# Performance work log

Hardware: AMD Instinct MI355X
Metric: run time of the kernel (lower is better)

## Reference

```python
import jax, jax.numpy as jnp
import numpy as np

N, NFEAT, NHID, NCLASS, H1 = 4096, 512, 64, 16, 8
GAIN = 1.414  # xavier gain used by the torch module
NEG_SLOPE = 0.2
MASK_VAL = -1e10


def _xavier(k, shape):
    fan_in, fan_out = shape[-2], shape[-1]
    lim = GAIN * (6.0 / (fan_in + fan_out)) ** 0.5
    return jax.random.uniform(k, shape, jnp.float32, -lim, lim)


def setup_inputs() -> dict:
    key = jax.random.key(0)
    ks = jax.random.split(key, 10)
    return {
        "x": jax.random.normal(ks[0], (N, NFEAT), jnp.float32),
        "adj": jax.random.randint(ks[1], (N, N), 0, 2, jnp.int32),
        # layer-1 parameters, stacked over H1 heads
        "W1": _xavier(ks[2], (H1, NFEAT, NHID)),
        "b1": jnp.zeros((H1, NHID), jnp.float32),
        "as1": _xavier(ks[3], (H1, NHID, 1))[..., 0],
        "an1": _xavier(ks[4], (H1, NHID, 1))[..., 0],
        # layer-2 parameters (single head, input = H1*NHID due to concat)
        "W2": _xavier(ks[5], (H1 * NHID, NCLASS)),
        "b2": jnp.zeros((NCLASS,), jnp.float32),
        "as2": _xavier(ks[6], (NCLASS, 1))[:, 0],
        "an2": _xavier(ks[7], (NCLASS, 1))[:, 0],
    }


def gat_layer(X, adj_pos, W, b, a_s, a_n):
    # X: [N, Fin], W: [Fin, Fout], a_s/a_n: [Fout], adj_pos: [N, N] bool
    feats = X @ W                                        # [N, Fout]
    s = feats @ a_s                                      # [N]
    nb = feats @ a_n                                     # [N]
    attn = jax.nn.leaky_relu(s[:, None] + nb[None, :], NEG_SLOPE)  # [N, N]
    attn = jnp.where(adj_pos, attn, MASK_VAL)
    attn = jax.nn.softmax(attn, axis=-1)
    # dropout on attn/feats is a no-op in eval mode
    return attn @ feats + b                              # [N, Fout]


def reference(x, adj, W1, b1, as1, an1, W2, b2, as2, an2):
    adj_pos = adj > 0
    # x dropout is a no-op in eval mode
    layer1 = jax.vmap(gat_layer, in_axes=(None, None, 0, 0, 0, 0))
    h = jax.nn.relu(layer1(x, adj_pos, W1, b1, as1, an1))    # [H1, N, NHID]
    h = jnp.transpose(h, (1, 0, 2)).reshape(N, H1 * NHID)    # concat heads on dim 1
    h = jax.nn.elu(h)
    out = jax.nn.relu(gat_layer(h, adj_pos, W2, b2, as2, an2))  # [N, NCLASS]
    return jax.nn.log_softmax(out, axis=1)
```

## Files before the change

### kernel.cpp

```cpp
#include <hip/hip_runtime.h>

#define NN 4096
#define NFEAT 512
#define NHID 64
#define H1 8
#define NCLS 16
#define BND 40.0f
#define VSTR 72

typedef short bf16x8 __attribute__((ext_vector_type(8)));
typedef float f32x4 __attribute__((ext_vector_type(4)));

__device__ __forceinline__ unsigned short f2bf(float f) {
    unsigned u = __float_as_uint(f);
    u += 0x7fffu + ((u >> 16) & 1u);
    return (unsigned short)(u >> 16);
}
__device__ __forceinline__ float leaky(float v) { return fmaxf(v, 0.2f * v); }
__device__ __forceinline__ unsigned pkbf(float lo, float hi) {
    return __builtin_amdgcn_perm(__float_as_uint(hi) + 0x8000u,
                                 __float_as_uint(lo) + 0x8000u, 0x07060302u);
}
__device__ __forceinline__ bf16x8 mk8(unsigned a, unsigned b, unsigned c, unsigned d) {
    union { unsigned u[4]; bf16x8 v; } cv;
    cv.u[0] = a; cv.u[1] = b; cv.u[2] = c; cv.u[3] = d; return cv.v;
}

__global__ __launch_bounds__(256)
void k_prep(const int* __restrict__ adj, unsigned long long* __restrict__ bits,
            const float* __restrict__ W1, unsigned short* __restrict__ w1f)
{
    __shared__ float wt[64][65];
    const int t = threadIdx.x, bx = blockIdx.x;
    if (bx < NN) {
        const int wv = t >> 6, lane = t & 63;
        const int* ap = adj + (size_t)bx * NN;
        for (int w = wv; w < 64; w += 4) {
            unsigned long long m = __ballot(ap[w * 64 + lane] > 0);
            if (lane == 0) bits[(size_t)bx * 64 + w] = m;
        }
        return;
    }
    const int kt = (bx - NN) & 7, h = (bx - NN) >> 3;
    #pragma unroll
    for (int i = 0; i < 4; ++i) {
        const int f = t + 256 * i;
        const int r = f >> 4, c4 = f & 15;
        const float4 v = *(const float4*)(W1 + ((size_t)(h * NFEAT) + kt * 64 + r) * NHID + c4 * 4);
        wt[r][c4 * 4 + 0] = v.x; wt[r][c4 * 4 + 1] = v.y;
        wt[r][c4 * 4 + 2] = v.z; wt[r][c4 * 4 + 3] = v.w;
    }
    __syncthreads();
    #pragma unroll
    for (int s = 0; s < 2; ++s) {
        const int o = t + s * 256;
        const int kg2 = o >> 8, rem = o & 255;
        const int nt = rem >> 6, lane2 = rem & 63;
        const int qq = lane2 >> 4, nn = lane2 & 15;
        const int kl = kg2 * 32 + qq * 8;
        const int c = nt * 16 + nn;
        uint4 w;
        w.x = pkbf(wt[kl + 0][c], wt[kl + 1][c]);
        w.y = pkbf(wt[kl + 2][c], wt[kl + 3][c]);
        w.z = pkbf(wt[kl + 4][c], wt[kl + 5][c]);
        w.w = pkbf(wt[kl + 6][c], wt[kl + 7][c]);
        *(uint4*)(w1f + (((size_t)h * 16 + kt * 2 + kg2) * 4 + nt) * 512 + lane2 * 8) = w;
    }
}

__global__ __launch_bounds__(256)
void k_feats1(const float* __restrict__ x, const unsigned short* __restrict__ w1f,
              const float* __restrict__ as1, const float* __restrict__ an1,
              unsigned short* __restrict__ f1bT, float* __restrict__ s1,
              float* __restrict__ F1a, float* __restrict__ F2a)
{
    const int t = threadIdx.x, wv = t >> 6, lane = t & 63;
    const int q = lane >> 4, n = lane & 15;
    const int h = blockIdx.y, R0 = blockIdx.x * 64;
    const int row = R0 + wv * 16 + n;
    const float* ap = x + (size_t)row * NFEAT;
    const unsigned short* wp = w1f + (size_t)h * 16 * 4 * 512 + lane * 8;
    f32x4 acc[4] = {{0.f,0.f,0.f,0.f},{0.f,0.f,0.f,0.f},{0.f,0.f,0.f,0.f},{0.f,0.f,0.f,0.f}};
    #pragma unroll 4
    for (int kg = 0; kg < 16; ++kg) {
        const float4 xa = *(const float4*)(ap + kg * 32 + q * 8);
        const float4 xb = *(const float4*)(ap + kg * 32 + q * 8 + 4);
        const bf16x8 af = mk8(pkbf(xa.x, xa.y), pkbf(xa.z, xa.w),
                              pkbf(xb.x, xb.y), pkbf(xb.z, xb.w));
        #pragma unroll
        for (int nt = 0; nt < 4; ++nt) {
            const bf16x8 bf = *(const bf16x8*)(wp + (size_t)(kg * 4 + nt) * 512);
            acc[nt] = __builtin_amdgcn_mfma_f32_16x16x32_bf16(af, bf, acc[nt], 0, 0, 0);
        }
    }
    #pragma unroll
    for (int nt = 0; nt < 4; ++nt) {
        uint2 w;
        w.x = pkbf(acc[nt][0], acc[nt][1]);
        w.y = pkbf(acc[nt][2], acc[nt][3]);
        *(uint2*)(f1bT + ((size_t)h * NHID + nt * 16 + n) * NN + R0 + wv * 16 + q * 4) = w;
    }
    float asv[4], anv[4];
    #pragma unroll
    for (int nt = 0; nt < 4; ++nt) {
        asv[nt] = as1[h * NHID + nt * 16 + n];
        anv[nt] = an1[h * NHID + nt * 16 + n];
    }
    #pragma unroll
    for (int i = 0; i < 4; ++i) {
        float ps = acc[0][i]*asv[0] + acc[1][i]*asv[1] + acc[2][i]*asv[2] + acc[3][i]*asv[3];
        float pn = acc[0][i]*anv[0] + acc[1][i]*anv[1] + acc[2][i]*anv[2] + acc[3][i]*anv[3];
        #pragma unroll
        for (int off = 8; off > 0; off >>= 1) {
            ps += __shfl_xor(ps, off, 64);
            pn += __shfl_xor(pn, off, 64);
        }
        if (n == 0) {
            const int idx = R0 + wv * 16 + q * 4 + i;
            s1[h * NN + idx] = ps;
            F1a[h * NN + idx] = __expf(pn - BND);
            F2a[h * NN + idx] = __expf(0.2f * (pn - BND));
        }
    }
}

__global__ __launch_bounds__(512, 4)
void k_gat1(const unsigned short* __restrict__ f1bT, const float* __restrict__ s1,
            const float* __restrict__ F1, const float* __restrict__ F2,
            const unsigned long long* __restrict__ abits, const float* __restrict__ b1,
            unsigned short* __restrict__ hcatb)
{
    __shared__ __align__(16) char smem[4 * 2 * 64 * VSTR * 2];
    unsigned short* vT = (unsigned short*)smem;

    const int t = threadIdx.x, wv = t >> 6, lane = t & 63;
    const int q = lane >> 4, n = lane & 15;
    const int rg = wv >> 2, jq = wv & 3;
    const int h = blockIdx.y, R0 = blockIdx.x * 64;
    const int rowA = R0 + rg * 32 + n;
    const int rowB = rowA + 16;
    const float vA = s1[h * NN + rowA] + BND, mhA = leaky(vA);
    const float vB = s1[h * NN + rowB] + BND, mhB = leaky(vB);
    const float E1A = __expf(vA - mhA), E2A = __expf(0.2f * vA - mhA);
    const float E1B = __expf(vB - mhB), E2B = __expf(0.2f * vB - mhB);
    const unsigned long long* arowA = abits + (size_t)rowA * 64;
    const unsigned long long* arowB = abits + (size_t)rowB * 64;
    const float* F1p = F1 + (size_t)h * NN;
    const float* F2p = F2 + (size_t)h * NN;

    const int stile = t >> 7;
    const int sc0 = (t & 127) >> 3, sj8 = t & 7;
    const unsigned short* sbase = f1bT + (size_t)h * NHID * NN + (size_t)sc0 * NN + sj8 * 8;
    const int dof = sc0 * VSTR + sj8 * 8;

    f32x4 accA[4] = {{0.f,0.f,0.f,0.f},{0.f,0.f,0.f,0.f},{0.f,0.f,0.f,0.f},{0.f,0.f,0.f,0.f}};
    f32x4 accB[4] = {{0.f,0.f,0.f,0.f},{0.f,0.f,0.f,0.f},{0.f,0.f,0.f,0.f},{0.f,0.f,0.f,0.f}};
    float lsA = 0.f, lsB = 0.f;

    {
        const int js = stile * 1024;
        int4 v0 = *(const int4*)(sbase + js);
        int4 v1 = *(const int4*)(sbase + (size_t)16 * NN + js);
        int4 v2 = *(const int4*)(sbase + (size_t)32 * NN + js);
        int4 v3 = *(const int4*)(sbase + (size_t)48 * NN + js);
        unsigned short* d = vT + (stile * 2 + 0) * (64 * VSTR) + dof;
        *(int4*)(d) = v0;
        *(int4*)(d + 16 * VSTR) = v1;
        *(int4*)(d + 32 * VSTR) = v2;
        *(int4*)(d + 48 * VSTR) = v3;
    }
    __syncthreads();

    for (int it = 0; it < 16; ++it) {
        const int db = it & 1;
        int4 p0, p1, p2, p3;
        if (it < 15) {
            const int js = stile * 1024 + (it + 1) * 64;
            p0 = *(const int4*)(sbase + js);
            p1 = *(const int4*)(sbase + (size_t)16 * NN + js);
            p2 = *(const int4*)(sbase + (size_t)32 * NN + js);
            p3 = *(const int4*)(sbase + (size_t)48 * NN + js);
        }
        const int j0 = jq * 1024 + it * 64;
        const unsigned long long aA = arowA[j0 >> 6];
        const unsigned long long aB = arowB[j0 >> 6];
        const unsigned short* tbase = vT + (jq * 2 + db) * (64 * VSTR);
        #pragma unroll
        for (int ch = 0; ch < 2; ++ch) {
            const int kb = ch * 32 + q * 8;
            const float4 f1a = *(const float4*)(F1p + j0 + kb);
            const float4 f1b = *(const float4*)(F1p + j0 + kb + 4);
            const float4 f2a = *(const float4*)(F2p + j0 + kb);
            const float4 f2b = *(const float4*)(F2p + j0 + kb + 4);
            const float F1v[8] = {f1a.x, f1a.y, f1a.z, f1a.w, f1b.x, f1b.y, f1b.z, f1b.w};
            const float F2v[8] = {f2a.x, f2a.y, f2a.z, f2a.w, f2b.x, f2b.y, f2b.z, f2b.w};
            const unsigned bA = (unsigned)(aA >> kb) & 0xffu;
            const unsigned bB = (unsigned)(aB >> kb) & 0xffu;
            unsigned uA[4], uB[4];
            #pragma unroll
            for (int jp = 0; jp < 4; ++jp) {
                float a0 = fmaxf(E1A * F1v[2*jp],   E2A * F2v[2*jp]);
                float a1 = fmaxf(E1A * F1v[2*jp+1], E2A * F2v[2*jp+1]);
                a0 = ((bA >> (2*jp)) & 1u) ? a0 : 0.f;
                a1 = ((bA >> (2*jp+1)) & 1u) ? a1 : 0.f;
                lsA += a0 + a1;
                uA[jp] = pkbf(a0, a1);
                float b0 = fmaxf(E1B * F1v[2*jp],   E2B * F2v[2*jp]);
                float b1v = fmaxf(E1B * F1v[2*jp+1], E2B * F2v[2*jp+1]);
                b0 = ((bB >> (2*jp)) & 1u) ? b0 : 0.f;
                b1v = ((bB >> (2*jp+1)) & 1u) ? b1v : 0.f;
                lsB += b0 + b1v;
                uB[jp] = pkbf(b0, b1v);
            }
            const bf16x8 afA = mk8(uA[0], uA[1], uA[2], uA[3]);
            const bf16x8 afB = mk8(uB[0], uB[1], uB[2], uB[3]);
            #pragma unroll
            for (int nt = 0; nt < 4; ++nt) {
                const bf16x8 bf = *(const bf16x8*)(tbase + (nt * 16 + n) * VSTR + kb);
                accA[nt] = __builtin_amdgcn_mfma_f32_16x16x32_bf16(afA, bf, accA[nt], 0, 0, 0);
                accB[nt] = __builtin_amdgcn_mfma_f32_16x16x32_bf16(afB, bf, accB[nt], 0, 0, 0);
            }
        }
        if (it < 15) {
            unsigned short* d = vT + (stile * 2 + (db ^ 1)) * (64 * VSTR) + dof;
            *(int4*)(d) = p0;
            *(int4*)(d + 16 * VSTR) = p1;
            *(int4*)(d + 32 * VSTR) = p2;
            *(int4*)(d + 48 * VSTR) = p3;
        }
        __syncthreads();
    }

    lsA += __shfl_xor(lsA, 16, 64); lsA += __shfl_xor(lsA, 32, 64);
    lsB += __shfl_xor(lsB, 16, 64); lsB += __shfl_xor(lsB, 32, 64);

    float* cmbf = (float*)smem;
    float* lwf  = (float*)(smem + 69632);
    #pragma unroll
    for (int nt = 0; nt < 4; ++nt)
        #pragma unroll
        for (int i = 0; i < 4; ++i) {
            cmbf[((size_t)jq * 64 + rg * 32 + q * 4 + i) * 68 + nt * 16 + n] = accA[nt][i];
            cmbf[((size_t)jq * 64 + rg * 32 + 16 + q * 4 + i) * 68 + nt * 16 + n] = accB[nt][i];
        }
    if (q == 0) {
        lwf[jq * 64 + rg * 32 + n] = lsA;
        lwf[jq * 64 + rg * 32 + 16 + n] = lsB;
    }
    __syncthreads();

    const int col = t & 63, r8 = t >> 6;
    const float bv = b1[h * NHID + col];
    #pragma unroll
    for (int rr = 0; rr < 8; ++rr) {
        const int r = r8 * 8 + rr;
        float tot = 0.f, lt = 0.f;
        #pragma unroll
        for (int jj = 0; jj < 4; ++jj) {
            tot += cmbf[((size_t)jj * 64 + r) * 68 + col];
            lt  += lwf[jj * 64 + r];
        }
        hcatb[(size_t)(R0 + r) * (H1 * NHID) + h * NHID + col] =
            f2bf(fmaxf(tot / lt + bv, 0.f));
    }
}

__global__ __launch_bounds__(128)
void k_feats2(const unsigned short* __restrict__ hcatb, const float* __restrict__ W2,
              const float* __restrict__ as2, const float* __restrict__ an2,
              unsigned short* __restrict__ f2bT, float* __restrict__ s2,
              float* __restrict__ F1b, float* __restrict__ F2b)
{
    __shared__ __align__(16) unsigned short w2T[NCLS][520];
    const int t = threadIdx.x, wv = t >> 6, lane = t & 63;
    const int q = lane >> 4, n = lane & 15;
    #pragma unroll
    for (int i = 0; i < 16; ++i) {
        const int f4 = t + 128 * i;
        const float4 v = ((const float4*)W2)[f4];
        const int k = f4 >> 2, c0 = (f4 & 3) * 4;
        w2T[c0 + 0][k] = f2bf(v.x); w2T[c0 + 1][k] = f2bf(v.y);
        w2T[c0 + 2][k] = f2bf(v.z); w2T[c0 + 3][k] = f2bf(v.w);
    }
    __syncthreads();

    const int R0 = blockIdx.x * 32;
    const int row = R0 + wv * 16 + n;
    const unsigned short* ap = hcatb + (size_t)row * NFEAT;
    f32x4 acc = {0.f, 0.f, 0.f, 0.f};
    #pragma unroll 4
    for (int k0 = 0; k0 < NFEAT; k0 += 32) {
        const bf16x8 af = *(const bf16x8*)(ap + k0 + q * 8);
        const bf16x8 bf = *(const bf16x8*)&w2T[n][k0 + q * 8];
        acc = __builtin_amdgcn_mfma_f32_16x16x32_bf16(af, bf, acc, 0, 0, 0);
    }
    uint2 w;
    w.x = pkbf(acc[0], acc[1]);
    w.y = pkbf(acc[2], acc[3]);
    *(uint2*)(f2bT + (size_t)n * NN + R0 + wv * 16 + q * 4) = w;
    const float asv = as2[n], anv = an2[n];
    #pragma unroll
    for (int i = 0; i < 4; ++i) {
        float ps = acc[i] * asv, pn = acc[i] * anv;
        #pragma unroll
        for (int off = 8; off > 0; off >>= 1) {
            ps += __shfl_xor(ps, off, 64);
            pn += __shfl_xor(pn, off, 64);
        }
        if (n == 0) {
            const int idx = R0 + wv * 16 + q * 4 + i;
            s2[idx] = ps;
            F1b[idx] = __expf(pn - BND);
            F2b[idx] = __expf(0.2f * (pn - BND));
        }
    }
}

__global__ __launch_bounds__(1024)
void k_gat2(const unsigned short* __restrict__ f2bT, const float* __restrict__ s2,
            const float* __restrict__ F1, const float* __restrict__ F2,
            const unsigned long long* __restrict__ abits, const float* __restrict__ b2,
            float* __restrict__ out)
{
    __shared__ float cmb[16][16][17];
    __shared__ float lw[16][16];
    const int t = threadIdx.x, wv = t >> 6, lane = t & 63;
    const int q = lane >> 4, n = lane & 15;
    const int R0 = blockIdx.x * 16, row = R0 + n;
    const float v = s2[row] + BND, mhat = leaky(v);
    const float E1 = __expf(v - mhat), E2 = __expf(0.2f * v - mhat);
    const unsigned long long* arow = abits + (size_t)row * 64;

    f32x4 acc = {0.f, 0.f, 0.f, 0.f};
    float lsum = 0.f;
    const int jbeg = wv * 256;
    for (int j0 = jbeg; j0 < jbeg + 256; j0 += 64) {
        const unsigned long long a64 = arow[j0 >> 6];
        #pragma unroll
        for (int ch = 0; ch < 2; ++ch) {
            const int kb = ch * 32 + q * 8;
            const float4 f1a = *(const float4*)(F1 + j0 + kb);
            const float4 f1b = *(const float4*)(F1 + j0 + kb + 4);
            const float4 f2a = *(const float4*)(F2 + j0 + kb);
            const float4 f2b = *(const float4*)(F2 + j0 + kb + 4);
            const float F1v[8] = {f1a.x, f1a.y, f1a.z, f1a.w, f1b.x, f1b.y, f1b.z, f1b.w};
            const float F2v[8] = {f2a.x, f2a.y, f2a.z, f2a.w, f2b.x, f2b.y, f2b.z, f2b.w};
            const unsigned b8 = (unsigned)(a64 >> kb) & 0xffu;
            unsigned au[4];
            #pragma unroll
            for (int jp = 0; jp < 4; ++jp) {
                float p0 = fmaxf(E1 * F1v[2*jp],   E2 * F2v[2*jp]);
                float p1 = fmaxf(E1 * F1v[2*jp+1], E2 * F2v[2*jp+1]);
                p0 = ((b8 >> (2*jp)) & 1u) ? p0 : 0.f;
                p1 = ((b8 >> (2*jp+1)) & 1u) ? p1 : 0.f;
                lsum += p0 + p1;
                au[jp] = pkbf(p0, p1);
            }
            const bf16x8 af = mk8(au[0], au[1], au[2], au[3]);
            const bf16x8 bf = *(const bf16x8*)(f2bT + (size_t)n * NN + j0 + kb);
            acc = __builtin_amdgcn_mfma_f32_16x16x32_bf16(af, bf, acc, 0, 0, 0);
        }
    }
    lsum += __shfl_xor(lsum, 16, 64);
    lsum += __shfl_xor(lsum, 32, 64);
    #pragma unroll
    for (int i = 0; i < 4; ++i) cmb[wv][q * 4 + i][n] = acc[i];
    if (q == 0) lw[wv][n] = lsum;
    __syncthreads();

    if (t < 256) {
        const int r = t >> 4, c = t & 15;
        float tot = 0.f, lt = 0.f;
        #pragma unroll
        for (int w16 = 0; w16 < 16; ++w16) { tot += cmb[w16][r][c]; lt += lw[w16][r]; }
        float val = fmaxf(tot / lt + b2[c], 0.f);
        float mx = val;
        #pragma unroll
        for (int off = 1; off < 16; off <<= 1) mx = fmaxf(mx, __shfl_xor(mx, off, 64));
        const float e = __expf(val - mx);
        float se = e;
        #pragma unroll
        for (int off = 1; off < 16; off <<= 1) se += __shfl_xor(se, off, 64);
        out[(size_t)(R0 + r) * NCLS + c] = val - mx - __logf(se);
    }
}

extern "C" void kernel_launch(void* const* d_in, const int* in_sizes, int n_in,
                              void* d_out, int out_size, void* d_ws, size_t ws_size,
                              hipStream_t stream)
{
    const float* x   = (const float*)d_in[0];
    const int*   adj = (const int*)  d_in[1];
    const float* W1  = (const float*)d_in[2];
    const float* b1  = (const float*)d_in[3];
    const float* as1 = (const float*)d_in[4];
    const float* an1 = (const float*)d_in[5];
    const float* W2  = (const float*)d_in[6];
    const float* b2  = (const float*)d_in[7];
    const float* as2 = (const float*)d_in[8];
    const float* an2 = (const float*)d_in[9];
    float* out = (float*)d_out;

    char* ws = (char*)d_ws;
    unsigned long long* abits = (unsigned long long*)(ws);
    unsigned short* f1bT  = (unsigned short*)(ws + (2u << 20));
    unsigned short* hcatb = (unsigned short*)(ws + (6u << 20));
    unsigned short* w1f   = (unsigned short*)(ws + (10u << 20));
    char* ws2 = ws + (10u << 20) + (512u << 10);
    float* s1   = (float*)(ws2);
    float* F1a  = (float*)(ws2 + (128u << 10));
    float* F2a  = (float*)(ws2 + (256u << 10));
    unsigned short* f2bT = (unsigned short*)(ws2 + (384u << 10));
    float* s2   = (float*)(ws2 + (512u << 10));
    float* F1b  = (float*)(ws2 + (528u << 10));
    float* F2b  = (float*)(ws2 + (544u << 10));

    k_prep  <<<dim3(NN + 64),     256, 0, stream>>>(adj, abits, W1, w1f);
    k_feats1<<<dim3(NN / 64, H1), 256, 0, stream>>>(x, w1f, as1, an1, f1bT, s1, F1a, F2a);
    k_gat1  <<<dim3(NN / 64, H1), 512, 0, stream>>>(f1bT, s1, F1a, F2a, abits, b1, hcatb);
    k_feats2<<<dim3(NN / 32),     128, 0, stream>>>(hcatb, W2, as2, an2, f2bT, s2, F1b, F2b);
    k_gat2  <<<dim3(NN / 16),     1024, 0, stream>>>(f2bT, s2, F1b, F2b, abits, b2, out);
}
```

Before: 209.8 us.

## Switch layer-1 attention to packed fp16 math with per-head max-shifted exponent factors

Layer 1 now uses fp16 instead of bf16 for inputs, weights, features and attention probabilities. It computes attention weights with packed half2 multiply/max and masks them by multiplying with 0/1 constants. x is converted to fp16 once in the prep kernel, and a new per-head kernel rescales the neighbour exponent factors by the per-head max and stores them as fp16 scaled by a constant. The aim is to halve the ALU work and load bandwidth in the inner attention loop and the global loads in the feature GEMM, at the cost of an extra small launch, reduced fp16 range and precision risk, and an 8-block kernel that runs with little parallelism.

```diff
diff --git a/kernel.cpp b/kernel.cpp
--- a/kernel.cpp
+++ b/kernel.cpp
@@ -7,8 +7,12 @@
 #define NCLS 16
 #define BND 40.0f
 #define VSTR 72
+#define FSCL 4096.0f
 
 typedef short bf16x8 __attribute__((ext_vector_type(8)));
+typedef _Float16 f16x8 __attribute__((ext_vector_type(8)));
+typedef _Float16 h2 __attribute__((ext_vector_type(2)));
+typedef __fp16 fp16v2 __attribute__((ext_vector_type(2)));
 typedef float f32x4 __attribute__((ext_vector_type(4)));
 
 __device__ __forceinline__ unsigned short f2bf(float f) {
@@ -21,14 +25,26 @@
     return __builtin_amdgcn_perm(__float_as_uint(hi) + 0x8000u,
                                  __float_as_uint(lo) + 0x8000u, 0x07060302u);
 }
+__device__ __forceinline__ unsigned pkh(float lo, float hi) {
+    union { fp16v2 h; unsigned u; } c;
+    c.h = __builtin_amdgcn_cvt_pkrtz(lo, hi);
+    return c.u;
+}
+__device__ __forceinline__ h2 uash(unsigned u) { union { unsigned u; h2 h; } c; c.u = u; return c.h; }
+__device__ __forceinline__ unsigned hasu(h2 h) { union { unsigned u; h2 h; } c; c.h = h; return c.u; }
 __device__ __forceinline__ bf16x8 mk8(unsigned a, unsigned b, unsigned c, unsigned d) {
     union { unsigned u[4]; bf16x8 v; } cv;
     cv.u[0] = a; cv.u[1] = b; cv.u[2] = c; cv.u[3] = d; return cv.v;
 }
+__device__ __forceinline__ f16x8 mk8h(unsigned a, unsigned b, unsigned c, unsigned d) {
+    union { unsigned u[4]; f16x8 v; } cv;
+    cv.u[0] = a; cv.u[1] = b; cv.u[2] = c; cv.u[3] = d; return cv.v;
+}
 
 __global__ __launch_bounds__(256)
 void k_prep(const int* __restrict__ adj, unsigned long long* __restrict__ bits,
-            const float* __restrict__ W1, unsigned short* __restrict__ w1f)
+            const float* __restrict__ W1, unsigned short* __restrict__ w1f,
+            const float* __restrict__ x, unsigned short* __restrict__ xh)
 {
     __shared__ float wt[64][65];
     const int t = threadIdx.x, bx = blockIdx.x;
@@ -41,6 +57,17 @@
         }
         return;
     }
+    if (bx >= NN + 64) {
+        const int b = bx - NN - 64;
+        #pragma unroll
+        for (int i = 0; i < 4; ++i) {
+            const int f4 = b * 1024 + i * 256 + t;
+            const float4 v = ((const float4*)x)[f4];
+            uint2 w; w.x = pkh(v.x, v.y); w.y = pkh(v.z, v.w);
+            ((uint2*)xh)[f4] = w;
+        }
+        return;
+    }
     const int kt = (bx - NN) & 7, h = (bx - NN) >> 3;
     #pragma unroll
     for (int i = 0; i < 4; ++i) {
@@ -60,44 +87,40 @@
         const int kl = kg2 * 32 + qq * 8;
         const int c = nt * 16 + nn;
         uint4 w;
-        w.x = pkbf(wt[kl + 0][c], wt[kl + 1][c]);
-        w.y = pkbf(wt[kl + 2][c], wt[kl + 3][c]);
-        w.z = pkbf(wt[kl + 4][c], wt[kl + 5][c]);
-        w.w = pkbf(wt[kl + 6][c], wt[kl + 7][c]);
+        w.x = pkh(wt[kl + 0][c], wt[kl + 1][c]);
+        w.y = pkh(wt[kl + 2][c], wt[kl + 3][c]);
+        w.z = pkh(wt[kl + 4][c], wt[kl + 5][c]);
+        w.w = pkh(wt[kl + 6][c], wt[kl + 7][c]);
         *(uint4*)(w1f + (((size_t)h * 16 + kt * 2 + kg2) * 4 + nt) * 512 + lane2 * 8) = w;
     }
 }
 
 __global__ __launch_bounds__(256)
-void k_feats1(const float* __restrict__ x, const unsigned short* __restrict__ w1f,
+void k_feats1(const unsigned short* __restrict__ xh, const unsigned short* __restrict__ w1f,
               const float* __restrict__ as1, const float* __restrict__ an1,
-              unsigned short* __restrict__ f1bT, float* __restrict__ s1,
-              float* __restrict__ F1a, float* __restrict__ F2a)
+              unsigned short* __restrict__ f1bT, float* __restrict__ s1, float* __restrict__ nb1)
 {
     const int t = threadIdx.x, wv = t >> 6, lane = t & 63;
     const int q = lane >> 4, n = lane & 15;
     const int h = blockIdx.y, R0 = blockIdx.x * 64;
     const int row = R0 + wv * 16 + n;
-    const float* ap = x + (size_t)row * NFEAT;
+    const unsigned short* ap = xh + (size_t)row * NFEAT;
     const unsigned short* wp = w1f + (size_t)h * 16 * 4 * 512 + lane * 8;
     f32x4 acc[4] = {{0.f,0.f,0.f,0.f},{0.f,0.f,0.f,0.f},{0.f,0.f,0.f,0.f},{0.f,0.f,0.f,0.f}};
     #pragma unroll 4
     for (int kg = 0; kg < 16; ++kg) {
-        const float4 xa = *(const float4*)(ap + kg * 32 + q * 8);
-        const float4 xb = *(const float4*)(ap + kg * 32 + q * 8 + 4);
-        const bf16x8 af = mk8(pkbf(xa.x, xa.y), pkbf(xa.z, xa.w),
-                              pkbf(xb.x, xb.y), pkbf(xb.z, xb.w));
+        const f16x8 af = *(const f16x8*)(ap + kg * 32 + q * 8);
         #pragma unroll
         for (int nt = 0; nt < 4; ++nt) {
-            const bf16x8 bf = *(const bf16x8*)(wp + (size_t)(kg * 4 + nt) * 512);
-            acc[nt] = __builtin_amdgcn_mfma_f32_16x16x32_bf16(af, bf, acc[nt], 0, 0, 0);
+            const f16x8 bf = *(const f16x8*)(wp + (size_t)(kg * 4 + nt) * 512);
+            acc[nt] = __builtin_amdgcn_mfma_f32_16x16x32_f16(af, bf, acc[nt], 0, 0, 0);
         }
     }
     #pragma unroll
     for (int nt = 0; nt < 4; ++nt) {
         uint2 w;
-        w.x = pkbf(acc[nt][0], acc[nt][1]);
-        w.y = pkbf(acc[nt][2], acc[nt][3]);
+        w.x = pkh(acc[nt][0], acc[nt][1]);
+        w.y = pkh(acc[nt][2], acc[nt][3]);
         *(uint2*)(f1bT + ((size_t)h * NHID + nt * 16 + n) * NN + R0 + wv * 16 + q * 4) = w;
     }
     float asv[4], anv[4];
@@ -118,17 +141,43 @@
         if (n == 0) {
             const int idx = R0 + wv * 16 + q * 4 + i;
             s1[h * NN + idx] = ps;
-            F1a[h * NN + idx] = __expf(pn - BND);
-            F2a[h * NN + idx] = __expf(0.2f * (pn - BND));
-        }
+            nb1[h * NN + idx] = pn;
+        }
+    }
+}
+
+__global__ __launch_bounds__(256)
+void k_fact1(const float* __restrict__ nb1, unsigned short* __restrict__ F1h,
+             unsigned short* __restrict__ F2h, float* __restrict__ nbmax)
+{
+    const int b = blockIdx.x, t = threadIdx.x;
+    const float* p = nb1 + (size_t)b * NN;
+    float m = -INFINITY;
+    for (int i = t; i < NN; i += 256) m = fmaxf(m, p[i]);
+    #pragma unroll
+    for (int off = 32; off > 0; off >>= 1) m = fmaxf(m, __shfl_xor(m, off, 64));
+    __shared__ float sm[4];
+    __shared__ float smx;
+    if ((t & 63) == 0) sm[t >> 6] = m;
+    __syncthreads();
+    if (t == 0) {
+        const float mm = fmaxf(fmaxf(sm[0], sm[1]), fmaxf(sm[2], sm[3]));
+        smx = mm; nbmax[b] = mm;
+    }
+    __syncthreads();
+    const float mx = smx;
+    for (int i = t * 2; i < NN; i += 512) {
+        const float d0 = p[i] - mx, d1 = p[i + 1] - mx;
+        ((unsigned*)F1h)[((size_t)b * NN + i) >> 1] = pkh(FSCL * __expf(d0), FSCL * __expf(d1));
+        ((unsigned*)F2h)[((size_t)b * NN + i) >> 1] = pkh(FSCL * __expf(0.2f * d0), FSCL * __expf(0.2f * d1));
     }
 }
 
 __global__ __launch_bounds__(512, 4)
 void k_gat1(const unsigned short* __restrict__ f1bT, const float* __restrict__ s1,
-            const float* __restrict__ F1, const float* __restrict__ F2,
+            const unsigned short* __restrict__ F1h, const unsigned short* __restrict__ F2h,
             const unsigned long long* __restrict__ abits, const float* __restrict__ b1,
-            unsigned short* __restrict__ hcatb)
+            const float* __restrict__ nbmax1, unsigned short* __restrict__ hcatb)
 {
     __shared__ __align__(16) char smem[4 * 2 * 64 * VSTR * 2];
     unsigned short* vT = (unsigned short*)smem;
@@ -139,14 +188,19 @@
     const int h = blockIdx.y, R0 = blockIdx.x * 64;
     const int rowA = R0 + rg * 32 + n;
     const int rowB = rowA + 16;
-    const float vA = s1[h * NN + rowA] + BND, mhA = leaky(vA);
-    const float vB = s1[h * NN + rowB] + BND, mhB = leaky(vB);
-    const float E1A = __expf(vA - mhA), E2A = __expf(0.2f * vA - mhA);
-    const float E1B = __expf(vB - mhB), E2B = __expf(0.2f * vB - mhB);
+    const float mh = nbmax1[h];
+    const float vA = s1[h * NN + rowA] + mh, mhA = leaky(vA);
+    const float vB = s1[h * NN + rowB] + mh, mhB = leaky(vB);
+    const float E1Af = __expf(vA - mhA), E2Af = __expf(0.2f * vA - mhA);
+    const float E1Bf = __expf(vB - mhB), E2Bf = __expf(0.2f * vB - mhB);
+    const h2 E1A = {(_Float16)E1Af, (_Float16)E1Af};
+    const h2 E2A = {(_Float16)E2Af, (_Float16)E2Af};
+    const h2 E1B = {(_Float16)E1Bf, (_Float16)E1Bf};
+    const h2 E2B = {(_Float16)E2Bf, (_Float16)E2Bf};
     const unsigned long long* arowA = abits + (size_t)rowA * 64;
     const unsigned long long* arowB = abits + (size_t)rowB * 64;
-    const float* F1p = F1 + (size_t)h * NN;
-    const float* F2p = F2 + (size_t)h * NN;
+    const unsigned short* F1p = F1h + (size_t)h * NN;
+    const unsigned short* F2p = F2h + (size_t)h * NN;
 
     const int stile = t >> 7;
     const int sc0 = (t & 127) >> 3, sj8 = t & 7;
@@ -188,37 +242,35 @@
         #pragma unroll
         for (int ch = 0; ch < 2; ++ch) {
             const int kb = ch * 32 + q * 8;
-            const float4 f1a = *(const float4*)(F1p + j0 + kb);
-            const float4 f1b = *(const float4*)(F1p + j0 + kb + 4);
-            const float4 f2a = *(const float4*)(F2p + j0 + kb);
-            const float4 f2b = *(const float4*)(F2p + j0 + kb + 4);
-            const float F1v[8] = {f1a.x, f1a.y, f1a.z, f1a.w, f1b.x, f1b.y, f1b.z, f1b.w};
-            const float F2v[8] = {f2a.x, f2a.y, f2a.z, f2a.w, f2b.x, f2b.y, f2b.z, f2b.w};
+            const uint4 f1w = *(const uint4*)(F1p + j0 + kb);
+            const uint4 f2w = *(const uint4*)(F2p + j0 + kb);
             const unsigned bA = (unsigned)(aA >> kb) & 0xffu;
             const unsigned bB = (unsigned)(aB >> kb) & 0xffu;
             unsigned uA[4], uB[4];
+            h2 sA2 = {(_Float16)0, (_Float16)0};
+            h2 sB2 = {(_Float16)0, (_Float16)0};
             #pragma unroll
             for (int jp = 0; jp < 4; ++jp) {
-                float a0 = fmaxf(E1A * F1v[2*jp],   E2A * F2v[2*jp]);
-                float a1 = fmaxf(E1A * F1v[2*jp+1], E2A * F2v[2*jp+1]);
-                a0 = ((bA >> (2*jp)) & 1u) ? a0 : 0.f;
-                a1 = ((bA >> (2*jp+1)) & 1u) ? a1 : 0.f;
-                lsA += a0 + a1;
-                uA[jp] = pkbf(a0, a1);
-                float b0 = fmaxf(E1B * F1v[2*jp],   E2B * F2v[2*jp]);
-                float b1v = fmaxf(E1B * F1v[2*jp+1], E2B * F2v[2*jp+1]);
-                b0 = ((bB >> (2*jp)) & 1u) ? b0 : 0.f;
-                b1v = ((bB >> (2*jp+1)) & 1u) ? b1v : 0.f;
-                lsB += b0 + b1v;
-                uB[jp] = pkbf(b0, b1v);
+                const h2 f1 = uash(((const unsigned*)&f1w)[jp]);
+                const h2 f2 = uash(((const unsigned*)&f2w)[jp]);
+                const unsigned mA = ((bA >> (2*jp)) & 1u) * 0x3C00u
+                                  + ((bA >> (2*jp+1)) & 1u) * 0x3C000000u;
+                const unsigned mB = ((bB >> (2*jp)) & 1u) * 0x3C00u
+                                  + ((bB >> (2*jp+1)) & 1u) * 0x3C000000u;
+                h2 pA = __builtin_elementwise_max(E1A * f1, E2A * f2) * uash(mA);
+                h2 pB = __builtin_elementwise_max(E1B * f1, E2B * f2) * uash(mB);
+                sA2 += pA; sB2 += pB;
+                uA[jp] = hasu(pA); uB[jp] = hasu(pB);
             }
-            const bf16x8 afA = mk8(uA[0], uA[1], uA[2], uA[3]);
-            const bf16x8 afB = mk8(uB[0], uB[1], uB[2], uB[3]);
+            lsA += (float)sA2[0] + (float)sA2[1];
+            lsB += (float)sB2[0] + (float)sB2[1];
+            const f16x8 afA = mk8h(uA[0], uA[1], uA[2], uA[3]);
+            const f16x8 afB = mk8h(uB[0], uB[1], uB[2], uB[3]);
             #pragma unroll
             for (int nt = 0; nt < 4; ++nt) {
-                const bf16x8 bf = *(const bf16x8*)(tbase + (nt * 16 + n) * VSTR + kb);
-                accA[nt] = __builtin_amdgcn_mfma_f32_16x16x32_bf16(afA, bf, accA[nt], 0, 0, 0);
-                accB[nt] = __builtin_amdgcn_mfma_f32_16x16x32_bf16(afB, bf, accB[nt], 0, 0, 0);
+                const f16x8 bf = *(const f16x8*)(tbase + (nt * 16 + n) * VSTR + kb);
+                accA[nt] = __builtin_amdgcn_mfma_f32_16x16x32_f16(afA, bf, accA[nt], 0, 0, 0);
+                accB[nt] = __builtin_amdgcn_mfma_f32_16x16x32_f16(afB, bf, accB[nt], 0, 0, 0);
             }
         }
         if (it < 15) {
@@ -404,20 +456,24 @@
     char* ws = (char*)d_ws;
     unsigned long long* abits = (unsigned long long*)(ws);
     unsigned short* f1bT  = (unsigned short*)(ws + (2u << 20));
-    unsigned short* hcatb = (unsigned short*)(ws + (6u << 20));
+    unsigned short* xh    = (unsigned short*)(ws + (6u << 20));
+    unsigned short* hcatb = xh;
     unsigned short* w1f   = (unsigned short*)(ws + (10u << 20));
     char* ws2 = ws + (10u << 20) + (512u << 10);
     float* s1   = (float*)(ws2);
-    float* F1a  = (float*)(ws2 + (128u << 10));
-    float* F2a  = (float*)(ws2 + (256u << 10));
+    float* nb1  = (float*)(ws2 + (128u << 10));
+    unsigned short* F1h = (unsigned short*)(ws2 + (256u << 10));
+    unsigned short* F2h = (unsigned short*)(ws2 + (320u << 10));
     unsigned short* f2bT = (unsigned short*)(ws2 + (384u << 10));
     float* s2   = (float*)(ws2 + (512u << 10));
     float* F1b  = (float*)(ws2 + (528u << 10));
     float* F2b  = (float*)(ws2 + (544u << 10));
-
-    k_prep  <<<dim3(NN + 64),     256, 0, stream>>>(adj, abits, W1, w1f);
-    k_feats1<<<dim3(NN / 64, H1), 256, 0, stream>>>(x, w1f, as1, an1, f1bT, s1, F1a, F2a);
-    k_gat1  <<<dim3(NN / 64, H1), 512, 0, stream>>>(f1bT, s1, F1a, F2a, abits, b1, hcatb);
-    k_feats2<<<dim3(NN / 32),     128, 0, stream>>>(hcatb, W2, as2, an2, f2bT, s2, F1b, F2b);
-    k_gat2  <<<dim3(NN / 16),     1024, 0, stream>>>(f2bT, s2, F1b, F2b, abits, b2, out);
-}
+    float* nbmax1 = (float*)(ws2 + (560u << 10));
+
+    k_prep  <<<dim3(NN + 64 + 512), 256, 0, stream>>>(adj, abits, W1, w1f, x, xh);
+    k_feats1<<<dim3(NN / 64, H1),   256, 0, stream>>>(xh, w1f, as1, an1, f1bT, s1, nb1);
+    k_fact1 <<<dim3(H1),            256, 0, stream>>>(nb1, F1h, F2h, nbmax1);
+    k_gat1  <<<dim3(NN / 64, H1),   512, 0, stream>>>(f1bT, s1, F1h, F2h, abits, b1, nbmax1, hcatb);
+    k_feats2<<<dim3(NN / 32),       128, 0, stream>>>(hcatb, W2, as2, an2, f2bT, s2, F1b, F2b);
+    k_gat2  <<<dim3(NN / 16),       1024, 0, stream>>>(f2bT, s2, F1b, F2b, abits, b2, out);
+}
```

After: 212.4 us. About the same (+1.2%).
